# Kernel optimization log

Measured on AMD Instinct MI355X. Metric: run time of the kernel, lower is better.

## Reference

```python
import jax, jax.numpy as jnp
import numpy as np

CUTOFF = 10.0
EPS_W = 1e-5
EPS_LN = 1e-5

def _silu(v):
    return v * jax.nn.sigmoid(v)

def setup_inputs() -> dict:
    key = jax.random.key(0)
    ks = jax.random.split(key, 12)
    N, E, H, R = 50000, 300000, 256, 64
    s = lambda fan_in: 1.0 / np.sqrt(fan_in)
    inp = {
        'x': jax.random.normal(ks[0], (N, H), jnp.float32),
        'edge_index': jax.random.randint(ks[1], (2, E), 0, N, jnp.int64 if jax.config.jax_enable_x64 else jnp.int32),
        'distances': jax.random.uniform(ks[2], (E,), jnp.float32) * CUTOFF,
        'centers': jnp.linspace(0.0, CUTOFF, R).astype(jnp.float32),
        'widths': jnp.full((R,), CUTOFF / R, jnp.float32),
        'rbf_w1': jax.random.normal(ks[3], (R, R), jnp.float32) * s(R),
        'rbf_b1': jnp.zeros((R,), jnp.float32),
        'rbf_w2': jax.random.normal(ks[4], (R, R), jnp.float32) * s(R),
        'rbf_b2': jnp.zeros((R,), jnp.float32),
        'filt_w1': jax.random.normal(ks[5], (R, H), jnp.float32) * s(R),
        'filt_b1': jnp.zeros((H,), jnp.float32),
        'filt_w2': jax.random.normal(ks[6], (H, H), jnp.float32) * s(H),
        'filt_b2': jnp.zeros((H,), jnp.float32),
        'filt_w3': jax.random.normal(ks[7], (H, H), jnp.float32) * s(H),
        'filt_b3': jnp.zeros((H,), jnp.float32),
        'node_w': jax.random.normal(ks[8], (H, H), jnp.float32) * s(H),
        'node_b': jnp.zeros((H,), jnp.float32),
        'ln_g': jnp.ones((H,), jnp.float32),
        'ln_b': jnp.zeros((H,), jnp.float32),
        'gate_w': jax.random.normal(ks[9], (H, H), jnp.float32) * s(H),
        'gate_b': jnp.zeros((H,), jnp.float32),
    }
    return inp

def reference(x, edge_index, distances, centers, widths,
              rbf_w1, rbf_b1, rbf_w2, rbf_b2,
              filt_w1, filt_b1, filt_w2, filt_b2, filt_w3, filt_b3,
              node_w, node_b, ln_g, ln_b, gate_w, gate_b):
    # LearnableRBF: envelope * gaussian basis, then 2-layer SiLU proj
    d = distances
    env = 0.5 * (jnp.cos(d * jnp.pi / CUTOFF) + 1.0) * (d < CUTOFF).astype(x.dtype)  # [E]
    rbf = jnp.exp(-0.5 * ((d[:, None] - centers) / (jnp.abs(widths) + EPS_W)) ** 2)   # [E,R]
    r = rbf * env[:, None]
    r = _silu(r @ rbf_w1 + rbf_b1) @ rbf_w2 + rbf_b2                                  # [E,R]
    # filter network: Lin-SiLU-Lin-SiLU-Lin
    W = _silu(r @ filt_w1 + filt_b1)
    W = _silu(W @ filt_w2 + filt_b2) @ filt_w3 + filt_b3                              # [E,H]
    # gather -> modulate -> scatter-add (CFConv messaging)
    row, col = edge_index[0], edge_index[1]
    msg = (x[col] @ node_w + node_b) * W                                              # [E,H]
    agg = jax.ops.segment_sum(msg, row, num_segments=x.shape[0])                      # [N,H]
    h = x + agg
    mu = jnp.mean(h, axis=-1, keepdims=True)
    var = jnp.var(h, axis=-1, keepdims=True)
    out = (h - mu) / jnp.sqrt(var + EPS_LN) * ln_g + ln_b
    return out * jax.nn.sigmoid(out @ gate_w + gate_b)
```

## Files before the change

### kernel.cpp

```cpp
#include <hip/hip_runtime.h>
#include <hip/hip_bf16.h>
#include <math.h>

typedef __attribute__((ext_vector_type(8))) short bf16x8;
typedef __attribute__((ext_vector_type(4))) float f32x4;
typedef unsigned short ushort_t;

constexpr float F_CUTOFF = 10.0f;
constexpr float F_EPS_W  = 1e-5f;
constexpr float F_EPS_LN = 1e-5f;
constexpr float F_PI     = 3.14159265358979323846f;

__device__ __forceinline__ float silu_f(float v)   { return v / (1.0f + __expf(-v)); }
__device__ __forceinline__ float sigmoid_f(float v){ return 1.0f / (1.0f + __expf(-v)); }

__device__ __forceinline__ ushort_t f2bf(float f) {
    union { __hip_bfloat16 h; ushort_t u; } v; v.h = __float2bfloat16(f); return v.u;
}
__device__ __forceinline__ float bf2f(ushort_t u) {
    union { unsigned u; float f; } v; v.u = ((unsigned)u) << 16; return v.f;
}

__global__ void count_kernel(const int* __restrict__ eidx, int* __restrict__ cnt, int E)
{
    int e = blockIdx.x * 256 + threadIdx.x;
    if (e < E) atomicAdd(&cnt[eidx[e]], 1);
}

__global__ __launch_bounds__(256)
void scan_sum_kernel(const int* __restrict__ cnt, int* __restrict__ part, int N, int range)
{
    __shared__ int red[256];
    int base = blockIdx.x * range;
    int s = 0;
    for (int i = threadIdx.x; i < range; i += 256) {
        int idx = base + i;
        if (idx < N) s += cnt[idx];
    }
    red[threadIdx.x] = s;
    __syncthreads();
    #pragma unroll
    for (int o = 128; o > 0; o >>= 1) {
        if (threadIdx.x < o) red[threadIdx.x] += red[threadIdx.x + o];
        __syncthreads();
    }
    if (threadIdx.x == 0) part[blockIdx.x] = red[0];
}

__global__ __launch_bounds__(256)
void scan_write_kernel(const int* __restrict__ part, int* __restrict__ cnt ,
                       int* __restrict__ start, int N, int range, int E)
{
    __shared__ int ex[256];
    int tid = threadIdx.x;
    int v = part[tid];
    ex[tid] = v;
    __syncthreads();
    for (int o = 1; o < 256; o <<= 1) {
        int add = (tid >= o) ? ex[tid - o] : 0;
        __syncthreads();
        ex[tid] += add;
        __syncthreads();
    }
    int run = ex[tid] - v;
    int base = tid * range;
    for (int i = 0; i < range; ++i) {
        int idx = base + i;
        if (idx < N) {
            int c = cnt[idx];
            start[idx] = run;
            cnt[idx] = run;
            run += c;
        }
    }
    if (tid == 0) start[N] = E;
}

__global__ void scatter_kernel(const int* __restrict__ eidx, const float* __restrict__ dist,
                               int* __restrict__ cursor,
                               int* __restrict__ colp, int* __restrict__ nodep,
                               float* __restrict__ distp, int E)
{
    int e = blockIdx.x * 256 + threadIdx.x;
    if (e < E) {
        int row = eidx[e];
        int s = atomicAdd(&cursor[row], 1);
        colp[s]  = eidx[E + e];
        nodep[s] = row;
        distp[s] = dist[e];
    }
}

__global__ void cvt_transpose_kernel(const float* __restrict__ in, ushort_t* __restrict__ out,
                                     int K, int N, int logK)
{
    int idx = blockIdx.x * 256 + threadIdx.x;
    if (idx >= K * N) return;
    int n = idx >> logK;
    int k = idx & (K - 1);
    out[idx] = f2bf(in[k * N + n]);
}

__global__ void combine_w_kernel(const float* __restrict__ w2, const float* __restrict__ fw1,
                                 ushort_t* __restrict__ out)
{
    int idx = blockIdx.x * 256 + threadIdx.x;
    int c = idx >> 6, j = idx & 63;
    float s = 0.f;
    #pragma unroll 8
    for (int n = 0; n < 64; ++n) s += w2[j * 64 + n] * fw1[n * 256 + c];
    out[idx] = f2bf(s);
}

__global__ void combine_b_kernel(const float* __restrict__ b2, const float* __restrict__ fw1,
                                 const float* __restrict__ fb1, float* __restrict__ out)
{
    int c = threadIdx.x;
    float s = fb1[c];
    #pragma unroll 8
    for (int n = 0; n < 64; ++n) s += b2[n] * fw1[n * 256 + c];
    out[c] = s;
}

__global__ __launch_bounds__(256)
void cast_bf16_kernel(const float* __restrict__ in, ushort_t* __restrict__ out, long n4)
{
    long i = (long)blockIdx.x * 256 + threadIdx.x;
    if (i >= n4) return;
    float4 v = reinterpret_cast<const float4*>(in)[i];
    ushort_t o[4] = {f2bf(v.x), f2bf(v.y), f2bf(v.z), f2bf(v.w)};
    *reinterpret_cast<uint2*>(out + i * 4) = *reinterpret_cast<uint2*>(o);
}

__global__ __launch_bounds__(256)
void gemm256_bf16_kernel(const float* __restrict__ A, const float* __restrict__ Wm,
                         const float* __restrict__ bias, ushort_t* __restrict__ out, int M)
{
    __shared__ float4 As4[64][64];
    const int t = threadIdx.x;
    const int row0 = blockIdx.x * 64;

    #pragma unroll
    for (int i = 0; i < 16; ++i) {
        int flat = t + i * 256;
        int r = flat >> 6, k4 = flat & 63;
        int row = row0 + r;
        float4 v = make_float4(0.f, 0.f, 0.f, 0.f);
        if (row < M) v = reinterpret_cast<const float4*>(A)[row * 64 + k4];
        As4[r][k4] = v;
    }
    __syncthreads();

    const int jt  = t & 31;
    const int et  = t >> 5;
    const int j04 = jt * 2;
    const int r0  = et * 8;

    float acc[8][8];
    #pragma unroll
    for (int r = 0; r < 8; ++r)
        #pragma unroll
        for (int c = 0; c < 8; ++c) acc[r][c] = 0.f;

    for (int k4 = 0; k4 < 64; ++k4) {
        float4 a4[8];
        #pragma unroll
        for (int r = 0; r < 8; ++r) a4[r] = As4[r0 + r][k4];
        #pragma unroll
        for (int q = 0; q < 4; ++q) {
            const int k = k4 * 4 + q;
            float4 b0 = reinterpret_cast<const float4*>(Wm)[k * 64 + j04];
            float4 b1 = reinterpret_cast<const float4*>(Wm)[k * 64 + j04 + 1];
            float bb[8] = {b0.x, b0.y, b0.z, b0.w, b1.x, b1.y, b1.z, b1.w};
            float av;
            #pragma unroll
            for (int r = 0; r < 8; ++r) {
                av = (q == 0) ? a4[r].x : (q == 1) ? a4[r].y : (q == 2) ? a4[r].z : a4[r].w;
                #pragma unroll
                for (int c = 0; c < 8; ++c) acc[r][c] = fmaf(av, bb[c], acc[r][c]);
            }
        }
    }

    float4 bv0 = reinterpret_cast<const float4*>(bias)[j04];
    float4 bv1 = reinterpret_cast<const float4*>(bias)[j04 + 1];
    float bb[8] = {bv0.x, bv0.y, bv0.z, bv0.w, bv1.x, bv1.y, bv1.z, bv1.w};

    #pragma unroll
    for (int r = 0; r < 8; ++r) {
        int row = row0 + r0 + r;
        if (row >= M) continue;
        ushort_t o8[8];
        #pragma unroll
        for (int c = 0; c < 8; ++c) o8[c] = f2bf(acc[r][c] + bb[c]);
        *reinterpret_cast<uint4*>(out + (size_t)row * 256 + jt * 8) = *reinterpret_cast<uint4*>(o8);
    }
}

__global__ __launch_bounds__(256)
void gate_gemm_kernel(const float* __restrict__ A, const float* __restrict__ Wm,
                      const float* __restrict__ bias, float* __restrict__ out, int M)
{
    __shared__ float4 As4[64][64];
    const int t = threadIdx.x;
    const int row0 = blockIdx.x * 64;

    #pragma unroll
    for (int i = 0; i < 16; ++i) {
        int flat = t + i * 256;
        int r = flat >> 6, k4 = flat & 63;
        int row = row0 + r;
        float4 v = make_float4(0.f, 0.f, 0.f, 0.f);
        if (row < M) v = reinterpret_cast<const float4*>(A)[row * 64 + k4];
        As4[r][k4] = v;
    }
    __syncthreads();

    const int jt  = t & 31;
    const int et  = t >> 5;
    const int j04 = jt * 2;
    const int r0  = et * 8;

    float acc[8][8];
    #pragma unroll
    for (int r = 0; r < 8; ++r)
        #pragma unroll
        for (int c = 0; c < 8; ++c) acc[r][c] = 0.f;

    for (int k4 = 0; k4 < 64; ++k4) {
        float4 a4[8];
        #pragma unroll
        for (int r = 0; r < 8; ++r) a4[r] = As4[r0 + r][k4];
        #pragma unroll
        for (int q = 0; q < 4; ++q) {
            const int k = k4 * 4 + q;
            float4 b0 = reinterpret_cast<const float4*>(Wm)[k * 64 + j04];
            float4 b1 = reinterpret_cast<const float4*>(Wm)[k * 64 + j04 + 1];
            float bb[8] = {b0.x, b0.y, b0.z, b0.w, b1.x, b1.y, b1.z, b1.w};
            float av;
            #pragma unroll
            for (int r = 0; r < 8; ++r) {
                av = (q == 0) ? a4[r].x : (q == 1) ? a4[r].y : (q == 2) ? a4[r].z : a4[r].w;
                #pragma unroll
                for (int c = 0; c < 8; ++c) acc[r][c] = fmaf(av, bb[c], acc[r][c]);
            }
        }
    }

    float4 bv0 = reinterpret_cast<const float4*>(bias)[j04];
    float4 bv1 = reinterpret_cast<const float4*>(bias)[j04 + 1];
    float bb[8] = {bv0.x, bv0.y, bv0.z, bv0.w, bv1.x, bv1.y, bv1.z, bv1.w};

    #pragma unroll
    for (int r = 0; r < 8; ++r) {
        int row = row0 + r0 + r;
        if (row >= M) continue;
        float4 a0 = As4[r0 + r][j04];
        float4 a1 = As4[r0 + r][j04 + 1];
        float aa[8] = {a0.x, a0.y, a0.z, a0.w, a1.x, a1.y, a1.z, a1.w};
        float o[8];
        #pragma unroll
        for (int c = 0; c < 8; ++c) o[c] = aa[c] * sigmoid_f(acc[r][c] + bb[c]);
        reinterpret_cast<float4*>(out)[row * 64 + j04]     = make_float4(o[0], o[1], o[2], o[3]);
        reinterpret_cast<float4*>(out)[row * 64 + j04 + 1] = make_float4(o[4], o[5], o[6], o[7]);
    }
}

__global__ __launch_bounds__(256, 4)
void rbf_t1_kernel(const float* __restrict__ distp,
                   const float* __restrict__ centers, const float* __restrict__ widths,
                   const ushort_t* __restrict__ Wt, const float* __restrict__ bias,
                   ushort_t* __restrict__ out, int M)
{
    __shared__ __align__(16) unsigned char sA[128 * 128];
    const int t = threadIdx.x;
    const int m0 = blockIdx.x * 128;
    const int w = t >> 6, lane = t & 63;
    const int g = lane >> 4, q = lane & 15;

    #pragma unroll
    for (int i = 0; i < 4; ++i) {
        int s = t + i * 256;
        int r = s >> 3, u = s & 7;
        int row = m0 + r;
        float d = (row < M) ? distp[row] : F_CUTOFF;
        float env = (d < F_CUTOFF) ? 0.5f * (__cosf(d * (F_PI / F_CUTOFF)) + 1.0f) : 0.0f;
        int c0 = (u ^ (r & 7)) * 8;
        ushort_t o[8];
        #pragma unroll
        for (int j = 0; j < 8; ++j) {
            int n = c0 + j;
            float wd = fabsf(widths[n]) + F_EPS_W;
            float z = (d - centers[n]) / wd;
            o[j] = f2bf(env * __expf(-0.5f * z * z));
        }
        *reinterpret_cast<uint4*>(sA + s * 16) = *reinterpret_cast<uint4*>(o);
    }
    __syncthreads();

    f32x4 acc[2][4];
    #pragma unroll
    for (int mt = 0; mt < 2; ++mt)
        #pragma unroll
        for (int nt = 0; nt < 4; ++nt) acc[mt][nt] = (f32x4){0.f, 0.f, 0.f, 0.f};

    #pragma unroll
    for (int kk = 0; kk < 2; ++kk) {
        bf16x8 b[4];
        #pragma unroll
        for (int nt = 0; nt < 4; ++nt) {
            int n = nt * 16 + q;
            b[nt] = *reinterpret_cast<const bf16x8*>(Wt + n * 64 + kk * 32 + g * 8);
        }
        bf16x8 a[2];
        #pragma unroll
        for (int mt = 0; mt < 2; ++mt) {
            int m = w * 32 + mt * 16 + q;
            int unit = (4 * kk + g) ^ (m & 7);
            a[mt] = *reinterpret_cast<const bf16x8*>(sA + m * 128 + unit * 16);
        }
        #pragma unroll
        for (int mt = 0; mt < 2; ++mt)
            #pragma unroll
            for (int nt = 0; nt < 4; ++nt)
                acc[mt][nt] = __builtin_amdgcn_mfma_f32_16x16x32_bf16(a[mt], b[nt], acc[mt][nt], 0, 0, 0);
    }
    __syncthreads();

    const bool evenq = (q & 1) == 0;
    #pragma unroll
    for (int nt = 0; nt < 4; ++nt) {
        int n0  = nt * 16 + q;
        int n_e = n0 & ~1;
        float2 bv = *reinterpret_cast<const float2*>(bias + n_e);
        #pragma unroll
        for (int mt = 0; mt < 2; ++mt) {
            float v[4], p[4];
            #pragma unroll
            for (int r = 0; r < 4; ++r) { v[r] = acc[mt][nt][r]; p[r] = __shfl_xor(v[r], 1, 64); }
            #pragma unroll
            for (int rr = 0; rr < 2; ++rr) {
                int r = evenq ? rr : (2 + rr);
                float lo = silu_f((evenq ? v[r] : p[r]) + bv.x);
                float hi = silu_f((evenq ? p[r] : v[r]) + bv.y);
                int m = w * 32 + mt * 16 + 4 * g + r;
                unsigned u = (unsigned)f2bf(lo) | ((unsigned)f2bf(hi) << 16);
                *reinterpret_cast<unsigned*>(sA + m * 128 + n_e * 2) = u;
            }
        }
    }
    __syncthreads();

    {
        int row = t >> 1, j = t & 1;
        if (m0 + row < M) {
            #pragma unroll
            for (int i = 0; i < 4; ++i) {
                uint4 v = *reinterpret_cast<const uint4*>(sA + row * 128 + (j * 4 + i) * 16);
                *reinterpret_cast<uint4*>(out + (size_t)(m0 + row) * 64 + (j * 4 + i) * 8) = v;
            }
        }
    }
}

__global__ __launch_bounds__(256, 4)
void gemm_k64n256_kernel(const ushort_t* __restrict__ A, const ushort_t* __restrict__ Wt,
                         const float* __restrict__ bias, ushort_t* __restrict__ out, int M)
{
    __shared__ __align__(16) unsigned char sA[64 * 128];
    __shared__ __align__(16) unsigned char obuf[32 * 512];
    const int t = threadIdx.x;
    const int m0 = blockIdx.x * 64;
    const int wn = t >> 6, lane = t & 63;
    const int g = lane >> 4, q = lane & 15;

    #pragma unroll
    for (int i = 0; i < 2; ++i) {
        int s = t + i * 256;
        int r = s >> 3, u = s & 7;
        int row = m0 + r; row = (row < M) ? row : (M - 1);
        uint4 v = *reinterpret_cast<const uint4*>(A + (size_t)row * 64 + ((u ^ (r & 7)) * 8));
        *reinterpret_cast<uint4*>(sA + s * 16) = v;
    }
    __syncthreads();

    f32x4 acc[4][4];
    #pragma unroll
    for (int mt = 0; mt < 4; ++mt)
        #pragma unroll
        for (int nt = 0; nt < 4; ++nt) acc[mt][nt] = (f32x4){0.f, 0.f, 0.f, 0.f};

    #pragma unroll
    for (int kk = 0; kk < 2; ++kk) {
        bf16x8 b[4];
        #pragma unroll
        for (int nt = 0; nt < 4; ++nt) {
            int n = wn * 64 + nt * 16 + q;
            b[nt] = *reinterpret_cast<const bf16x8*>(Wt + n * 64 + kk * 32 + g * 8);
        }
        bf16x8 a[4];
        #pragma unroll
        for (int mt = 0; mt < 4; ++mt) {
            int m = mt * 16 + q;
            int unit = (4 * kk + g) ^ (m & 7);
            a[mt] = *reinterpret_cast<const bf16x8*>(sA + m * 128 + unit * 16);
        }
        #pragma unroll
        for (int mt = 0; mt < 4; ++mt)
            #pragma unroll
            for (int nt = 0; nt < 4; ++nt)
                acc[mt][nt] = __builtin_amdgcn_mfma_f32_16x16x32_bf16(a[mt], b[nt], acc[mt][nt], 0, 0, 0);
    }

    const bool evenq = (q & 1) == 0;
    #pragma unroll
    for (int half = 0; half < 2; ++half) {
        #pragma unroll
        for (int mtl = 0; mtl < 2; ++mtl) {
            int mt = half * 2 + mtl;
            #pragma unroll
            for (int nt = 0; nt < 4; ++nt) {
                int n0  = wn * 64 + nt * 16 + q;
                int n_e = n0 & ~1;
                float2 bv = *reinterpret_cast<const float2*>(bias + n_e);
                float v[4], p[4];
                #pragma unroll
                for (int r = 0; r < 4; ++r) { v[r] = acc[mt][nt][r]; p[r] = __shfl_xor(v[r], 1, 64); }
                #pragma unroll
                for (int rr = 0; rr < 2; ++rr) {
                    int r = evenq ? rr : (2 + rr);
                    float lo = silu_f((evenq ? v[r] : p[r]) + bv.x);
                    float hi = silu_f((evenq ? p[r] : v[r]) + bv.y);
                    int ml = mtl * 16 + 4 * g + r;
                    unsigned u = (unsigned)f2bf(lo) | ((unsigned)f2bf(hi) << 16);
                    *reinterpret_cast<unsigned*>(obuf + ml * 512 + n_e * 2) = u;
                }
            }
        }
        __syncthreads();
        {
            int row = t >> 3, c = t & 7;
            int grow = m0 + half * 32 + row;
            if (grow < M) {
                #pragma unroll
                for (int i = 0; i < 4; ++i) {
                    uint4 v = *reinterpret_cast<const uint4*>(obuf + row * 512 + (c + 8 * i) * 16);
                    *reinterpret_cast<uint4*>(out + (size_t)grow * 256 + (c + 8 * i) * 8) = v;
                }
            }
        }
        __syncthreads();
    }
}

template<bool SILU>
__global__ __launch_bounds__(256, 4)
void gemm_k256_kernel(const ushort_t* __restrict__ A, const ushort_t* __restrict__ Wt,
                      const float* __restrict__ bias, ushort_t* __restrict__ out, int M)
{
    __shared__ __align__(16) unsigned char sbuf[2][8192];

    const int t  = threadIdx.x;
    const int m0 = blockIdx.x * 64;
    const int wn   = t >> 6;
    const int lane = t & 63;
    const int g = lane >> 4, q = lane & 15;

    const int s0r = t >> 3,         s0u = t & 7;
    const int s1r = (t + 256) >> 3, s1u = t & 7;
    const ushort_t* src0base = A + (size_t)((m0 + s0r < M) ? (m0 + s0r) : (M - 1)) * 256 + ((s0u ^ (s0r & 7)) * 8);
    const ushort_t* src1base = A + (size_t)((m0 + s1r < M) ? (m0 + s1r) : (M - 1)) * 256 + ((s1u ^ (s1r & 7)) * 8);

    uint4 p0 = *reinterpret_cast<const uint4*>(src0base);
    uint4 p1 = *reinterpret_cast<const uint4*>(src1base);
    *reinterpret_cast<uint4*>(&sbuf[0][t * 16])         = p0;
    *reinterpret_cast<uint4*>(&sbuf[0][(t + 256) * 16]) = p1;
    __syncthreads();

    f32x4 acc[4][4];
    #pragma unroll
    for (int mt = 0; mt < 4; ++mt)
        #pragma unroll
        for (int nt = 0; nt < 4; ++nt) acc[mt][nt] = (f32x4){0.f, 0.f, 0.f, 0.f};

    for (int kt = 0; kt < 4; ++kt) {
        const int cur = kt & 1;
        uint4 nx0, nx1;
        if (kt < 3) {
            nx0 = *reinterpret_cast<const uint4*>(src0base + (kt + 1) * 64);
            nx1 = *reinterpret_cast<const uint4*>(src1base + (kt + 1) * 64);
        }
        #pragma unroll
        for (int ks = 0; ks < 2; ++ks) {
            bf16x8 b[4];
            #pragma unroll
            for (int nt = 0; nt < 4; ++nt) {
                int n = wn * 64 + nt * 16 + q;
                b[nt] = *reinterpret_cast<const bf16x8*>(Wt + (size_t)n * 256 + kt * 64 + ks * 32 + g * 8);
            }
            bf16x8 a[4];
            #pragma unroll
            for (int mt = 0; mt < 4; ++mt) {
                int r = mt * 16 + q;
                int u = (ks * 4 + g) ^ (r & 7);
                a[mt] = *reinterpret_cast<const bf16x8*>(&sbuf[cur][r * 128 + u * 16]);
            }
            #pragma unroll
            for (int mt = 0; mt < 4; ++mt)
                #pragma unroll
                for (int nt = 0; nt < 4; ++nt)
                    acc[mt][nt] = __builtin_amdgcn_mfma_f32_16x16x32_bf16(a[mt], b[nt], acc[mt][nt], 0, 0, 0);
        }
        __syncthreads();
        if (kt < 3) {
            *reinterpret_cast<uint4*>(&sbuf[cur ^ 1][t * 16])         = nx0;
            *reinterpret_cast<uint4*>(&sbuf[cur ^ 1][(t + 256) * 16]) = nx1;
            __syncthreads();
        }
    }

    unsigned char* obuf = &sbuf[0][0];
    const bool evenq = (q & 1) == 0;
    #pragma unroll
    for (int half = 0; half < 2; ++half) {
        __syncthreads();
        #pragma unroll
        for (int mtl = 0; mtl < 2; ++mtl) {
            int mt = half * 2 + mtl;
            #pragma unroll
            for (int nt = 0; nt < 4; ++nt) {
                int n0  = wn * 64 + nt * 16 + q;
                int n_e = n0 & ~1;
                float2 bv = *reinterpret_cast<const float2*>(bias + n_e);
                float v[4], p[4];
                #pragma unroll
                for (int r = 0; r < 4; ++r) { v[r] = acc[mt][nt][r]; p[r] = __shfl_xor(v[r], 1, 64); }
                #pragma unroll
                for (int rr = 0; rr < 2; ++rr) {
                    int r = evenq ? rr : (2 + rr);
                    float lo = (evenq ? v[r] : p[r]) + bv.x;
                    float hi = (evenq ? p[r] : v[r]) + bv.y;
                    if (SILU) { lo = silu_f(lo); hi = silu_f(hi); }
                    int ml = mtl * 16 + 4 * g + r;
                    unsigned u = (unsigned)f2bf(lo) | ((unsigned)f2bf(hi) << 16);
                    *reinterpret_cast<unsigned*>(obuf + ml * 512 + n_e * 2) = u;
                }
            }
        }
        __syncthreads();
        {
            int row = t >> 3, c = t & 7;
            int grow = m0 + half * 32 + row;
            if (grow < M) {
                #pragma unroll
                for (int i = 0; i < 4; ++i) {
                    uint4 v = *reinterpret_cast<const uint4*>(obuf + row * 512 + (c + 8 * i) * 16);
                    *reinterpret_cast<uint4*>(out + (size_t)grow * 256 + (c + 8 * i) * 8) = v;
                }
            }
        }
    }
}

__global__ __launch_bounds__(256, 4)
void gate_mfma_kernel(const ushort_t* __restrict__ A, const ushort_t* __restrict__ Wt,
                      const float* __restrict__ bias, float* __restrict__ out, int M)
{
    __shared__ __align__(16) unsigned char sbuf[2][8192];
    __shared__ float obuf[16][260];

    const int t  = threadIdx.x;
    const int m0 = blockIdx.x * 64;
    const int wn   = t >> 6;
    const int lane = t & 63;
    const int g = lane >> 4, q = lane & 15;

    const int s0r = t >> 3,         s0u = t & 7;
    const int s1r = (t + 256) >> 3, s1u = t & 7;
    const ushort_t* src0base = A + (size_t)((m0 + s0r < M) ? (m0 + s0r) : (M - 1)) * 256 + ((s0u ^ (s0r & 7)) * 8);
    const ushort_t* src1base = A + (size_t)((m0 + s1r < M) ? (m0 + s1r) : (M - 1)) * 256 + ((s1u ^ (s1r & 7)) * 8);

    uint4 p0 = *reinterpret_cast<const uint4*>(src0base);
    uint4 p1 = *reinterpret_cast<const uint4*>(src1base);
    *reinterpret_cast<uint4*>(&sbuf[0][t * 16])         = p0;
    *reinterpret_cast<uint4*>(&sbuf[0][(t + 256) * 16]) = p1;
    __syncthreads();

    f32x4 acc[4][4];
    #pragma unroll
    for (int mt = 0; mt < 4; ++mt)
        #pragma unroll
        for (int nt = 0; nt < 4; ++nt) acc[mt][nt] = (f32x4){0.f, 0.f, 0.f, 0.f};

    for (int kt = 0; kt < 4; ++kt) {
        const int cur = kt & 1;
        uint4 nx0, nx1;
        if (kt < 3) {
            nx0 = *reinterpret_cast<const uint4*>(src0base + (kt + 1) * 64);
            nx1 = *reinterpret_cast<const uint4*>(src1base + (kt + 1) * 64);
        }
        #pragma unroll
        for (int ks = 0; ks < 2; ++ks) {
            bf16x8 b[4];
            #pragma unroll
            for (int nt = 0; nt < 4; ++nt) {
                int n = wn * 64 + nt * 16 + q;
                b[nt] = *reinterpret_cast<const bf16x8*>(Wt + (size_t)n * 256 + kt * 64 + ks * 32 + g * 8);
            }
            bf16x8 a[4];
            #pragma unroll
            for (int mt = 0; mt < 4; ++mt) {
                int r = mt * 16 + q;
                int u = (ks * 4 + g) ^ (r & 7);
                a[mt] = *reinterpret_cast<const bf16x8*>(&sbuf[cur][r * 128 + u * 16]);
            }
            #pragma unroll
            for (int mt = 0; mt < 4; ++mt)
                #pragma unroll
                for (int nt = 0; nt < 4; ++nt)
                    acc[mt][nt] = __builtin_amdgcn_mfma_f32_16x16x32_bf16(a[mt], b[nt], acc[mt][nt], 0, 0, 0);
        }
        __syncthreads();
        if (kt < 3) {
            *reinterpret_cast<uint4*>(&sbuf[cur ^ 1][t * 16])         = nx0;
            *reinterpret_cast<uint4*>(&sbuf[cur ^ 1][(t + 256) * 16]) = nx1;
            __syncthreads();
        }
    }

    float bn[4];
    #pragma unroll
    for (int nt = 0; nt < 4; ++nt) bn[nt] = bias[wn * 64 + nt * 16 + q];

    #pragma unroll
    for (int p = 0; p < 4; ++p) {
        #pragma unroll
        for (int nt = 0; nt < 4; ++nt) {
            int col = wn * 64 + nt * 16 + q;
            #pragma unroll
            for (int r = 0; r < 4; ++r) {
                int rl = 4 * g + r;
                obuf[rl][col] = sigmoid_f(acc[p][nt][r] + bn[nt]);
            }
        }
        __syncthreads();
        {
            int rl = t >> 4, c16 = t & 15;
            int grow = m0 + p * 16 + rl;
            if (grow < M) {
                float* orow = out + (size_t)grow * 256 + c16 * 16;
                #pragma unroll
                for (int i = 0; i < 4; ++i) {
                    float4 g4 = *reinterpret_cast<const float4*>(&obuf[rl][c16 * 16 + i * 4]);
                    float4 a4 = *reinterpret_cast<const float4*>(orow + i * 4);
                    a4.x *= g4.x; a4.y *= g4.y; a4.z *= g4.z; a4.w *= g4.w;
                    *reinterpret_cast<float4*>(orow + i * 4) = a4;
                }
            }
        }
        __syncthreads();
    }
}

__global__ __launch_bounds__(256, 3)
void fused_de_kernel(const ushort_t* A, const ushort_t* __restrict__ Wt2,
                     const float* __restrict__ b2,
                     const ushort_t* __restrict__ Wt3, const float* __restrict__ b3,
                     ushort_t* out, int M)
{
    __shared__ __align__(16) unsigned char sbuf[2][8192];
    __shared__ __align__(16) unsigned char f2l[64 * 512];

    const int t  = threadIdx.x;
    const int m0 = blockIdx.x * 64;
    const int wn   = t >> 6;
    const int lane = t & 63;
    const int g = lane >> 4, q = lane & 15;

    const int s0r = t >> 3,         s0u = t & 7;
    const int s1r = (t + 256) >> 3, s1u = t & 7;
    const ushort_t* src0base = A + (size_t)((m0 + s0r < M) ? (m0 + s0r) : (M - 1)) * 256 + ((s0u ^ (s0r & 7)) * 8);
    const ushort_t* src1base = A + (size_t)((m0 + s1r < M) ? (m0 + s1r) : (M - 1)) * 256 + ((s1u ^ (s1r & 7)) * 8);

    uint4 p0 = *reinterpret_cast<const uint4*>(src0base);
    uint4 p1 = *reinterpret_cast<const uint4*>(src1base);
    *reinterpret_cast<uint4*>(&sbuf[0][t * 16])         = p0;
    *reinterpret_cast<uint4*>(&sbuf[0][(t + 256) * 16]) = p1;
    __syncthreads();

    f32x4 acc[4][4];
    #pragma unroll
    for (int mt = 0; mt < 4; ++mt)
        #pragma unroll
        for (int nt = 0; nt < 4; ++nt) acc[mt][nt] = (f32x4){0.f, 0.f, 0.f, 0.f};

    for (int kt = 0; kt < 4; ++kt) {
        const int cur = kt & 1;
        uint4 nx0, nx1;
        if (kt < 3) {
            nx0 = *reinterpret_cast<const uint4*>(src0base + (kt + 1) * 64);
            nx1 = *reinterpret_cast<const uint4*>(src1base + (kt + 1) * 64);
        }
        #pragma unroll
        for (int ks = 0; ks < 2; ++ks) {
            bf16x8 b[4];
            #pragma unroll
            for (int nt = 0; nt < 4; ++nt) {
                int n = wn * 64 + nt * 16 + q;
                b[nt] = *reinterpret_cast<const bf16x8*>(Wt2 + (size_t)n * 256 + kt * 64 + ks * 32 + g * 8);
            }
            bf16x8 a[4];
            #pragma unroll
            for (int mt = 0; mt < 4; ++mt) {
                int r = mt * 16 + q;
                int u = (ks * 4 + g) ^ (r & 7);
                a[mt] = *reinterpret_cast<const bf16x8*>(&sbuf[cur][r * 128 + u * 16]);
            }
            #pragma unroll
            for (int mt = 0; mt < 4; ++mt)
                #pragma unroll
                for (int nt = 0; nt < 4; ++nt)
                    acc[mt][nt] = __builtin_amdgcn_mfma_f32_16x16x32_bf16(a[mt], b[nt], acc[mt][nt], 0, 0, 0);
        }
        __syncthreads();
        if (kt < 3) {
            *reinterpret_cast<uint4*>(&sbuf[cur ^ 1][t * 16])         = nx0;
            *reinterpret_cast<uint4*>(&sbuf[cur ^ 1][(t + 256) * 16]) = nx1;
            __syncthreads();
        }
    }

    const bool evenq = (q & 1) == 0;
    #pragma unroll
    for (int nt = 0; nt < 4; ++nt) {
        int n0  = wn * 64 + nt * 16 + q;
        int n_e = n0 & ~1;
        float2 bv = *reinterpret_cast<const float2*>(b2 + n_e);
        #pragma unroll
        for (int mt = 0; mt < 4; ++mt) {
            float v[4], p[4];
            #pragma unroll
            for (int r = 0; r < 4; ++r) { v[r] = acc[mt][nt][r]; p[r] = __shfl_xor(v[r], 1, 64); }
            #pragma unroll
            for (int rr = 0; rr < 2; ++rr) {
                int r = evenq ? rr : (2 + rr);
                float lo = silu_f((evenq ? v[r] : p[r]) + bv.x);
                float hi = silu_f((evenq ? p[r] : v[r]) + bv.y);
                int m = mt * 16 + 4 * g + r;
                unsigned u = (unsigned)f2bf(lo) | ((unsigned)f2bf(hi) << 16);
                int byte = m * 512 + (((n_e >> 3) ^ (m & 7)) << 4) + ((n_e & 7) * 2);
                *reinterpret_cast<unsigned*>(f2l + byte) = u;
            }
        }
    }
    __syncthreads();

    #pragma unroll
    for (int mt = 0; mt < 4; ++mt)
        #pragma unroll
        for (int nt = 0; nt < 4; ++nt) acc[mt][nt] = (f32x4){0.f, 0.f, 0.f, 0.f};

    #pragma unroll
    for (int kk = 0; kk < 8; ++kk) {
        bf16x8 b[4];
        #pragma unroll
        for (int nt = 0; nt < 4; ++nt) {
            int n = wn * 64 + nt * 16 + q;
            b[nt] = *reinterpret_cast<const bf16x8*>(Wt3 + (size_t)n * 256 + kk * 32 + g * 8);
        }
        bf16x8 a[4];
        #pragma unroll
        for (int mt = 0; mt < 4; ++mt) {
            int m = mt * 16 + q;
            int unit = (4 * kk + g) ^ (m & 7);
            a[mt] = *reinterpret_cast<const bf16x8*>(f2l + m * 512 + unit * 16);
        }
        #pragma unroll
        for (int mt = 0; mt < 4; ++mt)
            #pragma unroll
            for (int nt = 0; nt < 4; ++nt)
                acc[mt][nt] = __builtin_amdgcn_mfma_f32_16x16x32_bf16(a[mt], b[nt], acc[mt][nt], 0, 0, 0);
    }

    unsigned char* obuf = &sbuf[0][0];
    #pragma unroll
    for (int half = 0; half < 2; ++half) {
        __syncthreads();
        #pragma unroll
        for (int mtl = 0; mtl < 2; ++mtl) {
            int mt = half * 2 + mtl;
            #pragma unroll
            for (int nt = 0; nt < 4; ++nt) {
                int n0  = wn * 64 + nt * 16 + q;
                int n_e = n0 & ~1;
                float2 bv = *reinterpret_cast<const float2*>(b3 + n_e);
                float v[4], p[4];
                #pragma unroll
                for (int r = 0; r < 4; ++r) { v[r] = acc[mt][nt][r]; p[r] = __shfl_xor(v[r], 1, 64); }
                #pragma unroll
                for (int rr = 0; rr < 2; ++rr) {
                    int r = evenq ? rr : (2 + rr);
                    float lo = (evenq ? v[r] : p[r]) + bv.x;
                    float hi = (evenq ? p[r] : v[r]) + bv.y;
                    int ml = mtl * 16 + 4 * g + r;
                    unsigned u = (unsigned)f2bf(lo) | ((unsigned)f2bf(hi) << 16);
                    *reinterpret_cast<unsigned*>(obuf + ml * 512 + n_e * 2) = u;
                }
            }
        }
        __syncthreads();
        {
            int row = t >> 3, c = t & 7;
            int grow = m0 + half * 32 + row;
            if (grow < M) {
                #pragma unroll
                for (int i = 0; i < 4; ++i) {
                    uint4 v = *reinterpret_cast<const uint4*>(obuf + row * 512 + (c + 8 * i) * 16);
                    *reinterpret_cast<uint4*>(out + (size_t)grow * 256 + (c + 8 * i) * 8) = v;
                }
            }
        }
    }
}

__global__ __launch_bounds__(256)
void agg_ln_node_kernel(const ushort_t* __restrict__ Wf, const int* __restrict__ colp,
                        const int* __restrict__ start, const ushort_t* __restrict__ y,
                        const float* __restrict__ x,
                        const float* __restrict__ gg, const float* __restrict__ bb,
                        float* __restrict__ out0, ushort_t* __restrict__ out_bf, int N)
{
    int lane = threadIdx.x & 63;
    int n    = blockIdx.x * 4 + (threadIdx.x >> 6);
    if (n >= N) return;
    int s0 = start[n], s1 = start[n + 1];

    float4 hx = reinterpret_cast<const float4*>(x)[n * 64 + lane];
    float h0 = hx.x, h1 = hx.y, h2 = hx.z, h3 = hx.w;
    for (int s = s0; s < s1; ++s) {
        uint2 wv = *reinterpret_cast<const uint2*>(Wf + (size_t)s * 256 + lane * 4);
        int c = colp[s];
        uint2 yv = *reinterpret_cast<const uint2*>(y + (size_t)c * 256 + lane * 4);
        h0 += bf2f((ushort_t)(wv.x & 0xffff)) * bf2f((ushort_t)(yv.x & 0xffff));
        h1 += bf2f((ushort_t)(wv.x >> 16))    * bf2f((ushort_t)(yv.x >> 16));
        h2 += bf2f((ushort_t)(wv.y & 0xffff)) * bf2f((ushort_t)(yv.y & 0xffff));
        h3 += bf2f((ushort_t)(wv.y >> 16))    * bf2f((ushort_t)(yv.y >> 16));
    }

    float su = h0 + h1 + h2 + h3;
    float s2 = h0 * h0 + h1 * h1 + h2 * h2 + h3 * h3;
    #pragma unroll
    for (int off = 32; off > 0; off >>= 1) {
        su += __shfl_xor(su, off, 64);
        s2 += __shfl_xor(s2, off, 64);
    }
    float mu  = su * (1.0f / 256.0f);
    float var = s2 * (1.0f / 256.0f) - mu * mu;
    float inv = rsqrtf(var + F_EPS_LN);
    float4 gv = reinterpret_cast<const float4*>(gg)[lane];
    float4 bv = reinterpret_cast<const float4*>(bb)[lane];
    float4 o;
    o.x = (h0 - mu) * inv * gv.x + bv.x;
    o.y = (h1 - mu) * inv * gv.y + bv.y;
    o.z = (h2 - mu) * inv * gv.z + bv.z;
    o.w = (h3 - mu) * inv * gv.w + bv.w;
    reinterpret_cast<float4*>(out0)[n * 64 + lane] = o;
    ushort_t ob[4] = {f2bf(o.x), f2bf(o.y), f2bf(o.z), f2bf(o.w)};
    *reinterpret_cast<uint2*>(out_bf + (size_t)n * 256 + lane * 4) = *reinterpret_cast<uint2*>(ob);
}

__global__ __launch_bounds__(256)
void agg_node_kernel(const ushort_t* __restrict__ Wf, const int* __restrict__ colp,
                     const int* __restrict__ start, const ushort_t* __restrict__ y,
                     float* __restrict__ agg, int cs, int ce, int N)
{
    int lane = threadIdx.x & 63;
    int n    = blockIdx.x * 4 + (threadIdx.x >> 6);
    if (n >= N) return;
    int s0 = start[n], s1 = start[n + 1];
    if (s1 <= cs || s0 >= ce) return;
    int lo = (s0 > cs) ? s0 : cs;
    int hi = (s1 < ce) ? s1 : ce;

    float h0 = 0.f, h1 = 0.f, h2 = 0.f, h3 = 0.f;
    for (int s = lo; s < hi; ++s) {
        uint2 wv = *reinterpret_cast<const uint2*>(Wf + (size_t)(s - cs) * 256 + lane * 4);
        int c = colp[s];
        uint2 yv = *reinterpret_cast<const uint2*>(y + (size_t)c * 256 + lane * 4);
        h0 += bf2f((ushort_t)(wv.x & 0xffff)) * bf2f((ushort_t)(yv.x & 0xffff));
        h1 += bf2f((ushort_t)(wv.x >> 16))    * bf2f((ushort_t)(yv.x >> 16));
        h2 += bf2f((ushort_t)(wv.y & 0xffff)) * bf2f((ushort_t)(yv.y & 0xffff));
        h3 += bf2f((ushort_t)(wv.y >> 16))    * bf2f((ushort_t)(yv.y >> 16));
    }

    float* row = agg + (size_t)n * 256 + lane * 4;
    if (s0 >= cs && s1 <= ce) {
        *reinterpret_cast<float4*>(row) = make_float4(h0, h1, h2, h3);
    } else {
        unsafeAtomicAdd(&row[0], h0);
        unsafeAtomicAdd(&row[1], h1);
        unsafeAtomicAdd(&row[2], h2);
        unsafeAtomicAdd(&row[3], h3);
    }
}

template<int KS, int NT, bool SILU>
__device__ __forceinline__ void mlp_stage(const unsigned char* in, unsigned char* out,
                                          const ushort_t* __restrict__ Wt,
                                          const float* __restrict__ bias,
                                          int wn, int g, int q)
{
    constexpr int K = KS * 32;
    f32x4 acc[2][NT];
    #pragma unroll
    for (int mt = 0; mt < 2; ++mt)
        #pragma unroll
        for (int nt = 0; nt < NT; ++nt) acc[mt][nt] = (f32x4){0.f, 0.f, 0.f, 0.f};

    #pragma unroll
    for (int kk = 0; kk < KS; ++kk) {
        bf16x8 b[NT];
        #pragma unroll
        for (int nt = 0; nt < NT; ++nt) {
            int n = (wn * NT + nt) * 16 + q;
            b[nt] = *reinterpret_cast<const bf16x8*>(Wt + n * K + kk * 32 + g * 8);
        }
        bf16x8 a[2];
        #pragma unroll
        for (int mt = 0; mt < 2; ++mt) {
            int m = mt * 16 + q;
            int unit = (4 * kk + g) ^ (m & 7);
            a[mt] = *reinterpret_cast<const bf16x8*>(in + m * 512 + unit * 16);
        }
        #pragma unroll
        for (int mt = 0; mt < 2; ++mt)
            #pragma unroll
            for (int nt = 0; nt < NT; ++nt)
                acc[mt][nt] = __builtin_amdgcn_mfma_f32_16x16x32_bf16(a[mt], b[nt], acc[mt][nt], 0, 0, 0);
    }

    const bool evenq = (q & 1) == 0;
    #pragma unroll
    for (int nt = 0; nt < NT; ++nt) {
        int n0  = (wn * NT + nt) * 16 + q;
        int n_e = n0 & ~1;
        float2 bv = *reinterpret_cast<const float2*>(bias + n_e);
        #pragma unroll
        for (int mt = 0; mt < 2; ++mt) {
            float v[4], p[4];
            #pragma unroll
            for (int r = 0; r < 4; ++r) { v[r] = acc[mt][nt][r]; p[r] = __shfl_xor(v[r], 1, 64); }
            #pragma unroll
            for (int rr = 0; rr < 2; ++rr) {
                int r = evenq ? rr : (2 + rr);
                float lo = (evenq ? v[r] : p[r]) + bv.x;
                float hi = (evenq ? p[r] : v[r]) + bv.y;
                if (SILU) { lo = silu_f(lo); hi = silu_f(hi); }
                int m = mt * 16 + 4 * g + r;
                unsigned u = (unsigned)f2bf(lo) | ((unsigned)f2bf(hi) << 16);
                int byte = m * 512 + (((n_e >> 3) ^ (m & 7)) << 4) + ((n_e & 7) * 2);
                *reinterpret_cast<unsigned*>(out + byte) = u;
            }
        }
    }
}

__global__ __launch_bounds__(256, 4)
void edge_csr_kernel(const float* __restrict__ distp, const int* __restrict__ colp,
                     const int* __restrict__ nodep, const int* __restrict__ start,
                     const float* __restrict__ centers, const float* __restrict__ widths,
                     const ushort_t* __restrict__ wt_rbf1, const float* __restrict__ rbf_b1,
                     const ushort_t* __restrict__ wt_comb, const float* __restrict__ b_comb,
                     const ushort_t* __restrict__ wt_f2, const float* __restrict__ filt_b2,
                     const ushort_t* __restrict__ wt_f3, const float* __restrict__ filt_b3,
                     const ushort_t* __restrict__ y, float* __restrict__ agg, int E)
{
    __shared__ __align__(16) unsigned char buf[32768];
    __shared__ int node_s[32];
    __shared__ int flag_s[32];
    unsigned char* bufA = buf;
    unsigned char* bufB = buf + 16384;

    const int t  = threadIdx.x;
    const int e0 = blockIdx.x * 32;
    const int wn   = t >> 6;
    const int lane = t & 63;
    const int g = lane >> 4, q = lane & 15;

    if (t < 32) {
        int ge = e0 + t;
        int nd = (ge < E) ? nodep[ge] : -1;
        node_s[t] = nd;
        int fl = 0;
        if (nd >= 0) {
            int lo = start[nd], hi = start[nd + 1];
            fl = (lo >= e0 && hi <= e0 + 32) ? 1 : 0;
        }
        flag_s[t] = fl;
    }

    const int e_own  = t >> 3;
    const int chunk  = t & 7;
    const int ge_own = e0 + e_own;
    const int col_own = (ge_own < E) ? colp[ge_own] : 0;
    uint4 yv[4];
    #pragma unroll
    for (int i = 0; i < 4; ++i)
        yv[i] = *reinterpret_cast<const uint4*>(y + (size_t)col_own * 256 + (i * 8 + chunk) * 8);

    {
        float d = (ge_own < E) ? distp[ge_own] : F_CUTOFF;
        float env = (d < F_CUTOFF) ? 0.5f * (__cosf(d * (F_PI / F_CUTOFF)) + 1.0f) : 0.0f;
        unsigned char* rowp = bufA + e_own * 512;
        int k0 = chunk * 8;
        #pragma unroll
        for (int i = 0; i < 4; ++i) {
            int n = k0 + 2 * i;
            float c0 = centers[n],     w0 = fabsf(widths[n]) + F_EPS_W;
            float c1 = centers[n + 1], w1 = fabsf(widths[n + 1]) + F_EPS_W;
            float z0 = (d - c0) / w0, z1 = (d - c1) / w1;
            float r0 = env * __expf(-0.5f * z0 * z0);
            float r1 = env * __expf(-0.5f * z1 * z1);
            unsigned u = (unsigned)f2bf(r0) | ((unsigned)f2bf(r1) << 16);
            int byte = (((n >> 3) ^ (e_own & 7)) << 4) + ((n & 7) * 2);
            *reinterpret_cast<unsigned*>(rowp + byte) = u;
        }
    }
    __syncthreads();

    mlp_stage<2, 1, true>(bufA, bufB, wt_rbf1, rbf_b1, wn, g, q);
    __syncthreads();
    mlp_stage<2, 4, true>(bufB, bufA, wt_comb, b_comb, wn, g, q);
    __syncthreads();
    mlp_stage<8, 4, true>(bufA, bufB, wt_f2, filt_b2, wn, g, q);
    __syncthreads();

    #pragma unroll
    for (int i = 0; i < 4; ++i)
        *reinterpret_cast<uint4*>(bufA + e_own * 512 + (i * 8 + chunk) * 16) = yv[i];
    __syncthreads();

    f32x4 acc[2][4];
    #pragma unroll
    for (int mt = 0; mt < 2; ++mt)
        #pragma unroll
        for (int nt = 0; nt < 4; ++nt) acc[mt][nt] = (f32x4){0.f, 0.f, 0.f, 0.f};

    #pragma unroll
    for (int kk = 0; kk < 8; ++kk) {
        bf16x8 b[4];
        #pragma unroll
        for (int nt = 0; nt < 4; ++nt) {
            int n = (wn * 4 + nt) * 16 + q;
            b[nt] = *reinterpret_cast<const bf16x8*>(wt_f3 + n * 256 + kk * 32 + g * 8);
        }
        bf16x8 a[2];
        #pragma unroll
        for (int mt = 0; mt < 2; ++mt) {
            int m = mt * 16 + q;
            int unit = (4 * kk + g) ^ (m & 7);
            a[mt] = *reinterpret_cast<const bf16x8*>(bufB + m * 512 + unit * 16);
        }
        #pragma unroll
        for (int mt = 0; mt < 2; ++mt)
            #pragma unroll
            for (int nt = 0; nt < 4; ++nt)
                acc[mt][nt] = __builtin_amdgcn_mfma_f32_16x16x32_bf16(a[mt], b[nt], acc[mt][nt], 0, 0, 0);
    }

    float bn[4];
    int   nn[4];
    #pragma unroll
    for (int nt = 0; nt < 4; ++nt) { nn[nt] = (wn * 4 + nt) * 16 + q; bn[nt] = filt_b3[nn[nt]]; }

    #pragma unroll
    for (int mt = 0; mt < 2; ++mt) {
        #pragma unroll
        for (int r = 0; r < 4; ++r) {
            int m = mt * 16 + 4 * g + r;
            const unsigned char* yrow = bufA + m * 512;
            #pragma unroll
            for (int nt = 0; nt < 4; ++nt) {
                float yvv = bf2f(*reinterpret_cast<const ushort_t*>(yrow + nn[nt] * 2));
                acc[mt][nt][r] = (acc[mt][nt][r] + bn[nt]) * yvv;
            }
        }
    }
    __syncthreads();

    float* msgf = reinterpret_cast<float*>(buf);
    #pragma unroll
    for (int mt = 0; mt < 2; ++mt) {
        #pragma unroll
        for (int r = 0; r < 4; ++r) {
            int m = mt * 16 + 4 * g + r;
            #pragma unroll
            for (int nt = 0; nt < 4; ++nt)
                msgf[m * 256 + nn[nt]] = acc[mt][nt][r];
        }
    }
    __syncthreads();

    {
        const int j = t;
        float accv = 0.f;
        int cur = -2, rs = 0;
        #pragma unroll 4
        for (int r = 0; r < 32; ++r) {
            int nd = node_s[r];
            if (nd != cur) {
                if (cur >= 0) {
                    if (flag_s[rs]) agg[(size_t)cur * 256 + j] = accv;
                    else            unsafeAtomicAdd(&agg[(size_t)cur * 256 + j], accv);
                }
                cur = nd; rs = r; accv = msgf[r * 256 + j];
            } else {
                accv += msgf[r * 256 + j];
            }
        }
        if (cur >= 0) {
            if (flag_s[rs]) agg[(size_t)cur * 256 + j] = accv;
            else            unsafeAtomicAdd(&agg[(size_t)cur * 256 + j], accv);
        }
    }
}

__global__ __launch_bounds__(256)
void ln_kernel(const float* __restrict__ x, const float* __restrict__ agg,
               const float* __restrict__ g, const float* __restrict__ b,
               float* __restrict__ out0, ushort_t* __restrict__ out_bf, int N)
{
    int lane = threadIdx.x & 63;
    int row  = blockIdx.x * 4 + (threadIdx.x >> 6);
    if (row >= N) return;
    float4 hx = reinterpret_cast<const float4*>(x)[row * 64 + lane];
    float4 ha = reinterpret_cast<const float4*>(agg)[row * 64 + lane];
    float4 h  = make_float4(hx.x + ha.x, hx.y + ha.y, hx.z + ha.z, hx.w + ha.w);
    float s  = h.x + h.y + h.z + h.w;
    float s2 = h.x * h.x + h.y * h.y + h.z * h.z + h.w * h.w;
    #pragma unroll
    for (int off = 32; off > 0; off >>= 1) {
        s  += __shfl_xor(s,  off, 64);
        s2 += __shfl_xor(s2, off, 64);
    }
    float mu  = s * (1.0f / 256.0f);
    float var = s2 * (1.0f / 256.0f) - mu * mu;
    float inv = rsqrtf(var + F_EPS_LN);
    float4 gv = reinterpret_cast<const float4*>(g)[lane];
    float4 bv = reinterpret_cast<const float4*>(b)[lane];
    float4 o;
    o.x = (h.x - mu) * inv * gv.x + bv.x;
    o.y = (h.y - mu) * inv * gv.y + bv.y;
    o.z = (h.z - mu) * inv * gv.z + bv.z;
    o.w = (h.w - mu) * inv * gv.w + bv.w;
    reinterpret_cast<float4*>(out0)[row * 64 + lane] = o;
    ushort_t ob[4] = {f2bf(o.x), f2bf(o.y), f2bf(o.z), f2bf(o.w)};
    *reinterpret_cast<uint2*>(out_bf + (size_t)row * 256 + lane * 4) = *reinterpret_cast<uint2*>(ob);
}

extern "C" void kernel_launch(void* const* d_in, const int* in_sizes, int n_in,
                              void* d_out, int out_size, void* d_ws, size_t ws_size,
                              hipStream_t stream)
{
    const float* x       = (const float*)d_in[0];
    const int*   eidx    = (const int*)  d_in[1];
    const float* dist    = (const float*)d_in[2];
    const float* centers = (const float*)d_in[3];
    const float* widths  = (const float*)d_in[4];
    const float* rbf_w1  = (const float*)d_in[5];
    const float* rbf_b1  = (const float*)d_in[6];
    const float* rbf_w2  = (const float*)d_in[7];
    const float* rbf_b2  = (const float*)d_in[8];
    const float* filt_w1 = (const float*)d_in[9];
    const float* filt_b1 = (const float*)d_in[10];
    const float* filt_w2 = (const float*)d_in[11];
    const float* filt_b2 = (const float*)d_in[12];
    const float* filt_w3 = (const float*)d_in[13];
    const float* filt_b3 = (const float*)d_in[14];
    const float* node_w  = (const float*)d_in[15];
    const float* node_b  = (const float*)d_in[16];
    const float* ln_g    = (const float*)d_in[17];
    const float* ln_b    = (const float*)d_in[18];
    const float* gate_w  = (const float*)d_in[19];
    const float* gate_b  = (const float*)d_in[20];

    const int N = in_sizes[0] / 256;
    const int E = in_sizes[2];

    char* wsb = (char*)d_ws;
    size_t off = 0;
    auto alloc = [&](size_t bytes, size_t align) -> char* {
        off = (off + align - 1) & ~(align - 1);
        char* p = wsb + off;
        off += bytes;
        return p;
    };
    ushort_t* y_bf   = (ushort_t*)alloc((size_t)N * 256 * 2, 16);
    ushort_t* wt1    = (ushort_t*)alloc(64 * 64 * 2, 16);
    ushort_t* wcomb  = (ushort_t*)alloc(256 * 64 * 2, 16);
    ushort_t* wf2t   = (ushort_t*)alloc(256 * 256 * 2, 16);
    ushort_t* wf3t   = (ushort_t*)alloc(256 * 256 * 2, 16);
    ushort_t* wnodet = (ushort_t*)alloc(256 * 256 * 2, 16);
    ushort_t* wgatet = (ushort_t*)alloc(256 * 256 * 2, 16);
    float*    bcomb  = (float*)   alloc(256 * 4, 16);
    int*      part   = (int*)     alloc(256 * 4, 16);
    int*      cnt    = (int*)     alloc((size_t)N * 4, 16);
    int*      start  = (int*)     alloc(((size_t)N + 1) * 4, 16);
    int*      colp   = (int*)     alloc((size_t)E * 4, 16);
    int*      nodep  = (int*)     alloc((size_t)E * 4, 16);
    float*    distp  = (float*)   alloc((size_t)E * 4, 256);

    size_t fixed_off = (off + 1023) & ~(size_t)1023;
    size_t avail = (ws_size > fixed_off) ? (ws_size - fixed_off) : 0;
    long Rl = (long)(avail / 640);
    int R = (int)(Rl & ~127L);
    int Eround = (E + 127) & ~127;
    if (R > Eround) R = Eround;
    const bool dense = (R >= 128) && ((E + R - 1) / R <= 8)
                       && ((size_t)R * 640 >= (size_t)N * 512 + 1024);
    const int nchunks = dense ? ((E + R - 1) / R) : 0;
    ushort_t* rt_buf = (ushort_t*)(wsb + fixed_off);
    ushort_t* fw_buf = rt_buf + (size_t)R * 64;
    ushort_t* x_bf   = rt_buf;
    ushort_t* a_bf   = rt_buf;

    dim3 b256(256);
    const int range = (N + 255) / 256;

    cvt_transpose_kernel<<<dim3((64 * 64 + 255) / 256),   b256, 0, stream>>>(rbf_w1,  wt1, 64, 64, 6);
    combine_w_kernel<<<dim3(64), b256, 0, stream>>>(rbf_w2, filt_w1, wcomb);
    combine_b_kernel<<<dim3(1), b256, 0, stream>>>(rbf_b2, filt_w1, filt_b1, bcomb);
    cvt_transpose_kernel<<<dim3((256 * 256 + 255) / 256), b256, 0, stream>>>(filt_w2, wf2t, 256, 256, 8);
    cvt_transpose_kernel<<<dim3((256 * 256 + 255) / 256), b256, 0, stream>>>(filt_w3, wf3t, 256, 256, 8);
    cvt_transpose_kernel<<<dim3((256 * 256 + 255) / 256), b256, 0, stream>>>(node_w,  wnodet, 256, 256, 8);
    cvt_transpose_kernel<<<dim3((256 * 256 + 255) / 256), b256, 0, stream>>>(gate_w,  wgatet, 256, 256, 8);

    hipMemsetAsync(cnt, 0, (size_t)N * 4, stream);

    if (dense) {
        cast_bf16_kernel<<<dim3((N * 64 + 255) / 256), b256, 0, stream>>>(x, x_bf, (long)N * 64);
        gemm_k256_kernel<false><<<dim3((N + 63) / 64), b256, 0, stream>>>(
            x_bf, wnodet, node_b, y_bf, N);
    } else {
        gemm256_bf16_kernel<<<dim3((N + 63) / 64), b256, 0, stream>>>(x, node_w, node_b, y_bf, N);
    }

    count_kernel<<<dim3((E + 255) / 256), b256, 0, stream>>>(eidx, cnt, E);
    scan_sum_kernel<<<dim3(256), b256, 0, stream>>>(cnt, part, N, range);
    scan_write_kernel<<<dim3(1), b256, 0, stream>>>(part, cnt, start, N, range, E);
    scatter_kernel<<<dim3((E + 255) / 256), b256, 0, stream>>>(eidx, dist, cnt, colp, nodep, distp, E);

    if (dense) {
        if (nchunks > 1)
            hipMemsetAsync(d_out, 0, (size_t)out_size * sizeof(float), stream);

        for (int cs = 0; cs < E; cs += R) {
            int Mc = (E - cs < R) ? (E - cs) : R;
            rbf_t1_kernel<<<dim3((Mc + 127) / 128), b256, 0, stream>>>(
                distp + cs, centers, widths, wt1, rbf_b1, rt_buf, Mc);
            gemm_k64n256_kernel<<<dim3((Mc + 63) / 64), b256, 0, stream>>>(
                rt_buf, wcomb, bcomb, fw_buf, Mc);
            fused_de_kernel<<<dim3((Mc + 63) / 64), b256, 0, stream>>>(
                fw_buf, wf2t, filt_b2, wf3t, filt_b3, fw_buf, Mc);
            if (nchunks == 1) {
                agg_ln_node_kernel<<<dim3((N + 3) / 4), b256, 0, stream>>>(
                    fw_buf, colp, start, y_bf, x, ln_g, ln_b, (float*)d_out, a_bf, N);
            } else {
                agg_node_kernel<<<dim3((N + 3) / 4), b256, 0, stream>>>(
                    fw_buf, colp, start, y_bf, (float*)d_out, cs, cs + Mc, N);
            }
        }
        if (nchunks > 1) {
            ln_kernel<<<dim3((N + 3) / 4), b256, 0, stream>>>(
                x, (float*)d_out, ln_g, ln_b, (float*)d_out, a_bf, N);
        }
        gate_mfma_kernel<<<dim3((N + 63) / 64), b256, 0, stream>>>(
            a_bf, wgatet, gate_b, (float*)d_out, N);
    } else {
        hipMemsetAsync(d_out, 0, (size_t)out_size * sizeof(float), stream);
        edge_csr_kernel<<<dim3((E + 31) / 32), b256, 0, stream>>>(
            distp, colp, nodep, start, centers, widths,
            wt1, rbf_b1, wcomb, bcomb,
            wf2t, filt_b2, wf3t, filt_b3,
            y_bf, (float*)d_out, E);
        ln_kernel<<<dim3((N + 3) / 4), b256, 0, stream>>>(
            x, (float*)d_out, ln_g, ln_b, (float*)d_out, y_bf, N);
        gate_gemm_kernel<<<dim3((N + 63) / 64), b256, 0, stream>>>(
            (float*)d_out, gate_w, gate_b, (float*)d_out, N);
    }
}
```

Before: 853.3 us.

## Stage full K=256 A tile in LDS once instead of double-buffered K chunks

```diff
diff --git a/kernel.cpp b/kernel.cpp
--- a/kernel.cpp
+++ b/kernel.cpp
@@ -453,12 +453,26 @@
     }
 }
 
+__device__ __forceinline__ void stage_full_a(const ushort_t* A, unsigned char* al,
+                                             int m0, int M, int t)
+{
+    #pragma unroll
+    for (int i = 0; i < 8; ++i) {
+        int s = t + i * 256;
+        int r = s >> 5, u = s & 31;
+        int row = m0 + r; row = (row < M) ? row : (M - 1);
+        int c = (u & 24) | ((u ^ (r & 7)) & 7);
+        uint4 v = *reinterpret_cast<const uint4*>(A + (size_t)row * 256 + c * 8);
+        *reinterpret_cast<uint4*>(al + s * 16) = v;
+    }
+}
+
 template<bool SILU>
 __global__ __launch_bounds__(256, 4)
 void gemm_k256_kernel(const ushort_t* __restrict__ A, const ushort_t* __restrict__ Wt,
                       const float* __restrict__ bias, ushort_t* __restrict__ out, int M)
 {
-    __shared__ __align__(16) unsigned char sbuf[2][8192];
+    __shared__ __align__(16) unsigned char al[64 * 512];
 
     const int t  = threadIdx.x;
     const int m0 = blockIdx.x * 64;
@@ -466,15 +480,7 @@
     const int lane = t & 63;
     const int g = lane >> 4, q = lane & 15;
 
-    const int s0r = t >> 3,         s0u = t & 7;
-    const int s1r = (t + 256) >> 3, s1u = t & 7;
-    const ushort_t* src0base = A + (size_t)((m0 + s0r < M) ? (m0 + s0r) : (M - 1)) * 256 + ((s0u ^ (s0r & 7)) * 8);
-    const ushort_t* src1base = A + (size_t)((m0 + s1r < M) ? (m0 + s1r) : (M - 1)) * 256 + ((s1u ^ (s1r & 7)) * 8);
-
-    uint4 p0 = *reinterpret_cast<const uint4*>(src0base);
-    uint4 p1 = *reinterpret_cast<const uint4*>(src1base);
-    *reinterpret_cast<uint4*>(&sbuf[0][t * 16])         = p0;
-    *reinterpret_cast<uint4*>(&sbuf[0][(t + 256) * 16]) = p1;
+    stage_full_a(A, al, m0, M, t);
     __syncthreads();
 
     f32x4 acc[4][4];
@@ -483,43 +489,29 @@
         #pragma unroll
         for (int nt = 0; nt < 4; ++nt) acc[mt][nt] = (f32x4){0.f, 0.f, 0.f, 0.f};
 
-    for (int kt = 0; kt < 4; ++kt) {
-        const int cur = kt & 1;
-        uint4 nx0, nx1;
-        if (kt < 3) {
-            nx0 = *reinterpret_cast<const uint4*>(src0base + (kt + 1) * 64);
-            nx1 = *reinterpret_cast<const uint4*>(src1base + (kt + 1) * 64);
-        }
-        #pragma unroll
-        for (int ks = 0; ks < 2; ++ks) {
-            bf16x8 b[4];
-            #pragma unroll
-            for (int nt = 0; nt < 4; ++nt) {
-                int n = wn * 64 + nt * 16 + q;
-                b[nt] = *reinterpret_cast<const bf16x8*>(Wt + (size_t)n * 256 + kt * 64 + ks * 32 + g * 8);
-            }
-            bf16x8 a[4];
-            #pragma unroll
-            for (int mt = 0; mt < 4; ++mt) {
-                int r = mt * 16 + q;
-                int u = (ks * 4 + g) ^ (r & 7);
-                a[mt] = *reinterpret_cast<const bf16x8*>(&sbuf[cur][r * 128 + u * 16]);
-            }
-            #pragma unroll
-            for (int mt = 0; mt < 4; ++mt)
-                #pragma unroll
-                for (int nt = 0; nt < 4; ++nt)
-                    acc[mt][nt] = __builtin_amdgcn_mfma_f32_16x16x32_bf16(a[mt], b[nt], acc[mt][nt], 0, 0, 0);
-        }
-        __syncthreads();
-        if (kt < 3) {
-            *reinterpret_cast<uint4*>(&sbuf[cur ^ 1][t * 16])         = nx0;
-            *reinterpret_cast<uint4*>(&sbuf[cur ^ 1][(t + 256) * 16]) = nx1;
-            __syncthreads();
-        }
-    }
-
-    unsigned char* obuf = &sbuf[0][0];
+    #pragma unroll
+    for (int kk = 0; kk < 8; ++kk) {
+        bf16x8 b[4];
+        #pragma unroll
+        for (int nt = 0; nt < 4; ++nt) {
+            int n = wn * 64 + nt * 16 + q;
+            b[nt] = *reinterpret_cast<const bf16x8*>(Wt + (size_t)n * 256 + kk * 32 + g * 8);
+        }
+        bf16x8 a[4];
+        #pragma unroll
+        for (int mt = 0; mt < 4; ++mt) {
+            int r = mt * 16 + q;
+            int unit = (kk >> 1) * 8 + ((((kk & 1) * 4 + g) ^ (r & 7)));
+            a[mt] = *reinterpret_cast<const bf16x8*>(al + r * 512 + unit * 16);
+        }
+        #pragma unroll
+        for (int mt = 0; mt < 4; ++mt)
+            #pragma unroll
+            for (int nt = 0; nt < 4; ++nt)
+                acc[mt][nt] = __builtin_amdgcn_mfma_f32_16x16x32_bf16(a[mt], b[nt], acc[mt][nt], 0, 0, 0);
+    }
+
+    unsigned char* obuf = al;
     const bool evenq = (q & 1) == 0;
     #pragma unroll
     for (int half = 0; half < 2; ++half) {
@@ -662,13 +654,13 @@
     }
 }
 
-__global__ __launch_bounds__(256, 3)
+__global__ __launch_bounds__(256, 2)
 void fused_de_kernel(const ushort_t* A, const ushort_t* __restrict__ Wt2,
                      const float* __restrict__ b2,
                      const ushort_t* __restrict__ Wt3, const float* __restrict__ b3,
                      ushort_t* out, int M)
 {
-    __shared__ __align__(16) unsigned char sbuf[2][8192];
+    __shared__ __align__(16) unsigned char al[64 * 512];
     __shared__ __align__(16) unsigned char f2l[64 * 512];
 
     const int t  = threadIdx.x;
@@ -677,15 +669,7 @@
     const int lane = t & 63;
     const int g = lane >> 4, q = lane & 15;
 
-    const int s0r = t >> 3,         s0u = t & 7;
-    const int s1r = (t + 256) >> 3, s1u = t & 7;
-    const ushort_t* src0base = A + (size_t)((m0 + s0r < M) ? (m0 + s0r) : (M - 1)) * 256 + ((s0u ^ (s0r & 7)) * 8);
-    const ushort_t* src1base = A + (size_t)((m0 + s1r < M) ? (m0 + s1r) : (M - 1)) * 256 + ((s1u ^ (s1r & 7)) * 8);
-
-    uint4 p0 = *reinterpret_cast<const uint4*>(src0base);
-    uint4 p1 = *reinterpret_cast<const uint4*>(src1base);
-    *reinterpret_cast<uint4*>(&sbuf[0][t * 16])         = p0;
-    *reinterpret_cast<uint4*>(&sbuf[0][(t + 256) * 16]) = p1;
+    stage_full_a(A, al, m0, M, t);
     __syncthreads();
 
     f32x4 acc[4][4];
@@ -694,40 +678,26 @@
         #pragma unroll
         for (int nt = 0; nt < 4; ++nt) acc[mt][nt] = (f32x4){0.f, 0.f, 0.f, 0.f};
 
-    for (int kt = 0; kt < 4; ++kt) {
-        const int cur = kt & 1;
-        uint4 nx0, nx1;
-        if (kt < 3) {
-            nx0 = *reinterpret_cast<const uint4*>(src0base + (kt + 1) * 64);
-            nx1 = *reinterpret_cast<const uint4*>(src1base + (kt + 1) * 64);
-        }
-        #pragma unroll
-        for (int ks = 0; ks < 2; ++ks) {
-            bf16x8 b[4];
-            #pragma unroll
-            for (int nt = 0; nt < 4; ++nt) {
-                int n = wn * 64 + nt * 16 + q;
-                b[nt] = *reinterpret_cast<const bf16x8*>(Wt2 + (size_t)n * 256 + kt * 64 + ks * 32 + g * 8);
-            }
-            bf16x8 a[4];
-            #pragma unroll
-            for (int mt = 0; mt < 4; ++mt) {
-                int r = mt * 16 + q;
-                int u = (ks * 4 + g) ^ (r & 7);
-                a[mt] = *reinterpret_cast<const bf16x8*>(&sbuf[cur][r * 128 + u * 16]);
-            }
-            #pragma unroll
-            for (int mt = 0; mt < 4; ++mt)
-                #pragma unroll
-                for (int nt = 0; nt < 4; ++nt)
-                    acc[mt][nt] = __builtin_amdgcn_mfma_f32_16x16x32_bf16(a[mt], b[nt], acc[mt][nt], 0, 0, 0);
-        }
-        __syncthreads();
-        if (kt < 3) {
-            *reinterpret_cast<uint4*>(&sbuf[cur ^ 1][t * 16])         = nx0;
-            *reinterpret_cast<uint4*>(&sbuf[cur ^ 1][(t + 256) * 16]) = nx1;
-            __syncthreads();
-        }
+    #pragma unroll
+    for (int kk = 0; kk < 8; ++kk) {
+        bf16x8 b[4];
+        #pragma unroll
+        for (int nt = 0; nt < 4; ++nt) {
+            int n = wn * 64 + nt * 16 + q;
+            b[nt] = *reinterpret_cast<const bf16x8*>(Wt2 + (size_t)n * 256 + kk * 32 + g * 8);
+        }
+        bf16x8 a[4];
+        #pragma unroll
+        for (int mt = 0; mt < 4; ++mt) {
+            int r = mt * 16 + q;
+            int unit = (kk >> 1) * 8 + ((((kk & 1) * 4 + g) ^ (r & 7)));
+            a[mt] = *reinterpret_cast<const bf16x8*>(al + r * 512 + unit * 16);
+        }
+        #pragma unroll
+        for (int mt = 0; mt < 4; ++mt)
+            #pragma unroll
+            for (int nt = 0; nt < 4; ++nt)
+                acc[mt][nt] = __builtin_amdgcn_mfma_f32_16x16x32_bf16(a[mt], b[nt], acc[mt][nt], 0, 0, 0);
     }
 
     const bool evenq = (q & 1) == 0;
@@ -782,7 +752,7 @@
                 acc[mt][nt] = __builtin_amdgcn_mfma_f32_16x16x32_bf16(a[mt], b[nt], acc[mt][nt], 0, 0, 0);
     }
 
-    unsigned char* obuf = &sbuf[0][0];
+    unsigned char* obuf = al;
     #pragma unroll
     for (int half = 0; half < 2; ++half) {
         __syncthreads();
```

Result: no change. 864.5 us (+1.3%).
